# Performance work log

Measured on AMD Instinct MI355X. Metric: run time of the kernel, lower is better.

Reference implementation:

```python
import jax, jax.numpy as jnp
import numpy as np

B, S, D = 2, 2048, 2048
H, KVH = 32, 8
HD = D // H          # 64
N_REP = H // KVH     # 4
NEG = -1e9


def setup_inputs() -> dict:
    key = jax.random.key(0)
    ks = jax.random.split(key, 5)
    x = jax.random.normal(ks[0], (B, S, D), dtype=jnp.float32)
    std = 0.02
    wq = jax.random.normal(ks[1], (H * HD, D), dtype=jnp.float32) * std
    wk = jax.random.normal(ks[2], (KVH * HD, D), dtype=jnp.float32) * std
    wv = jax.random.normal(ks[3], (KVH * HD, D), dtype=jnp.float32) * std
    wo = jax.random.normal(ks[4], (D, H * HD), dtype=jnp.float32) * std
    # RoPE tables: (S, HD//2)
    inv_freq = 1.0 / (10000.0 ** (np.arange(0, HD, 2, dtype=np.float32) / HD))
    t = np.arange(S, dtype=np.float32)
    freqs = np.outer(t, inv_freq)
    freqs_cos = jnp.asarray(np.cos(freqs))
    freqs_sin = jnp.asarray(np.sin(freqs))
    # additive causal mask [1,1,S,S]
    causal = np.tril(np.ones((S, S), dtype=bool))
    mask = jnp.asarray(np.where(causal, 0.0, NEG).astype(np.float32))[None, None]
    return {"x": x, "wq": wq, "wk": wk, "wv": wv, "wo": wo,
            "freqs_cos": freqs_cos, "freqs_sin": freqs_sin, "mask": mask}


def _apply_rope(t, cos, sin):
    # t: [B,S,nh,HD]; cos/sin: [S, HD//2]
    tr = t.reshape(t.shape[:-1] + (HD // 2, 2))
    r, i = tr[..., 0], tr[..., 1]
    c = cos[None, :, None, :]
    s = sin[None, :, None, :]
    out_r = r * c - i * s
    out_i = r * s + i * c
    return jnp.stack([out_r, out_i], axis=-1).reshape(t.shape)


def reference(x, wq, wk, wv, wo, freqs_cos, freqs_sin, mask):
    b, s, _ = x.shape
    q = (x @ wq.T).reshape(b, s, H, HD)
    k = (x @ wk.T).reshape(b, s, KVH, HD)
    v = (x @ wv.T).reshape(b, s, KVH, HD)
    q = _apply_rope(q, freqs_cos, freqs_sin)
    k = _apply_rope(k, freqs_cos, freqs_sin)
    # repeat_kv (GQA expansion) then move heads forward: [B,H,S,HD]
    k = jnp.repeat(k, N_REP, axis=2)
    v = jnp.repeat(v, N_REP, axis=2)
    q = q.transpose(0, 2, 1, 3)
    k = k.transpose(0, 2, 1, 3)
    v = v.transpose(0, 2, 1, 3)
    scale = 1.0 / jnp.sqrt(jnp.float32(HD))
    scores = jnp.einsum("bhqd,bhkd->bhqk", q, k) * scale + mask[:, :, :s, :s]
    attn = jax.nn.softmax(scores, axis=-1)
    out = jnp.einsum("bhqk,bhkd->bhqd", attn, v)
    out = out.transpose(0, 2, 1, 3).reshape(b, s, H * HD)
    return out @ wo.T
```

## Files before the change

### kernel.cpp

```cpp
#include <hip/hip_runtime.h>
#include <hip/hip_bf16.h>
#include <stdint.h>


#define NEG_BIG (-1e9f)
#define SCALE_LOG2 0.18033688011112042f
#define DEFER_THR 10.0f

typedef __bf16 bf16x8 __attribute__((ext_vector_type(8)));
typedef float f32x4 __attribute__((ext_vector_type(4)));
typedef float f32x16 __attribute__((ext_vector_type(16)));
typedef uint16_t u16x8 __attribute__((ext_vector_type(8)));
typedef uint32_t u32x4 __attribute__((ext_vector_type(4)));

__device__ inline uint16_t f2bf(float x) {
    __hip_bfloat16 h = __float2bfloat16(x);
    return __builtin_bit_cast(uint16_t, h);
}
__device__ inline float bf2f(uint16_t u) {
    uint32_t t = (uint32_t)u << 16;
    return __builtin_bit_cast(float, t);
}

__device__ inline void async_cp16(const void* g, void* l) {
    __builtin_amdgcn_global_load_lds(
        (const __attribute__((address_space(1))) uint32_t*)g,
        (__attribute__((address_space(3))) uint32_t*)l,
        16 , 0 , 0 );
}

__global__ void cvt4(const float* __restrict__ in, uint16_t* __restrict__ out, int n4) {
    int i = blockIdx.x * blockDim.x + threadIdx.x;
    if (i >= n4) return;
    const float4 v = ((const float4*)in)[i];
    ushort4 o;
    o.x = f2bf(v.x); o.y = f2bf(v.y); o.z = f2bf(v.z); o.w = f2bf(v.w);
    ((ushort4*)out)[i] = o;
}

__global__ void build_wqkv(const float* __restrict__ wq, const float* __restrict__ wk,
                           const float* __restrict__ wv, uint16_t* __restrict__ out) {
    int i = blockIdx.x * blockDim.x + threadIdx.x;
    if (i >= (3072 * 2048) / 4) return;
    int e = i * 4;
    int row = e >> 11;
    int col = e & 2047;
    const float* src = (row < 2048) ? (wq + (long)row * 2048 + col)
                     : (row < 2560) ? (wk + (long)(row - 2048) * 2048 + col)
                                    : (wv + (long)(row - 2560) * 2048 + col);
    const float4 v = *(const float4*)src;
    ushort4 o;
    o.x = f2bf(v.x); o.y = f2bf(v.y); o.z = f2bf(v.z); o.w = f2bf(v.w);
    ((ushort4*)(out + e))[0] = o;
}

template <int OUT_BF16>
__global__ __launch_bounds__(256) void gemm_bt(const uint16_t* __restrict__ A,
                                               const uint16_t* __restrict__ Bw,
                                               void* __restrict__ Cout,
                                               int M, int N, int K) {
    __shared__ __align__(16) uint16_t Asm[128 * 32];
    __shared__ __align__(16) uint16_t Bsm[128 * 32];
    const int t = threadIdx.x;
    const int l = t & 63;
    const int w = t >> 6;
    const int wr = w >> 1, wc = w & 1;
    const int c = l & 15, g = l >> 4;
    const long row0 = (long)blockIdx.x * 128;
    const long col0 = (long)blockIdx.y * 128;

    f32x4 acc[4][4] = {};

    const uint16_t* aSrc = A + (row0 + (t >> 2)) * (long)K + (t & 3) * 8;
    const uint16_t* bSrc = Bw + (col0 + (t >> 2)) * (long)K + (t & 3) * 8;
    const long half = 64L * K;

    for (int k0 = 0; k0 < K; k0 += 32) {
        __syncthreads();
        async_cp16(aSrc + k0, &Asm[t * 8]);
        async_cp16(aSrc + half + k0, &Asm[2048 + t * 8]);
        async_cp16(bSrc + k0, &Bsm[t * 8]);
        async_cp16(bSrc + half + k0, &Bsm[2048 + t * 8]);
        __syncthreads();

        bf16x8 aF[4], bF[4];
        const int ko = g * 8;
#pragma unroll
        for (int m = 0; m < 4; ++m)
            aF[m] = *(const bf16x8*)&Asm[(wr * 64 + m * 16 + c) * 32 + ko];
#pragma unroll
        for (int n = 0; n < 4; ++n)
            bF[n] = *(const bf16x8*)&Bsm[(wc * 64 + n * 16 + c) * 32 + ko];
#pragma unroll
        for (int m = 0; m < 4; ++m)
#pragma unroll
            for (int n = 0; n < 4; ++n)
                acc[m][n] = __builtin_amdgcn_mfma_f32_16x16x32_bf16(aF[m], bF[n], acc[m][n], 0, 0, 0);
    }

#pragma unroll
    for (int m = 0; m < 4; ++m) {
        const long rg = row0 + wr * 64 + m * 16 + g * 4;
#pragma unroll
        for (int n = 0; n < 4; ++n) {
            const long cg = col0 + wc * 64 + n * 16 + c;
#pragma unroll
            for (int r = 0; r < 4; ++r) {
                float v = acc[m][n][r];
                if (OUT_BF16)
                    ((uint16_t*)Cout)[(rg + r) * (long)N + cg] = f2bf(v);
                else
                    ((float*)Cout)[(rg + r) * (long)N + cg] = v;
            }
        }
    }
}

__global__ void rope_q(uint16_t* __restrict__ qkv,
                       const float* __restrict__ cosT,
                       const float* __restrict__ sinT) {
    int idx = blockIdx.x * blockDim.x + threadIdx.x;
    if (idx >= 4096 * 1024) return;
    int m = idx >> 10;
    int j = idx & 1023;
    int s = m & 2047;
    int d2 = j & 31;
    float cc = cosT[s * 32 + d2];
    float ss = sinT[s * 32 + d2];
    uint32_t* p = (uint32_t*)(qkv + (long)m * 3072 + 2 * j);
    uint32_t v = *p;
    float re = bf2f((uint16_t)(v & 0xffffu));
    float im = bf2f((uint16_t)(v >> 16));
    float orr = re * cc - im * ss;
    float oi = re * ss + im * cc;
    *p = (uint32_t)f2bf(orr) | ((uint32_t)f2bf(oi) << 16);
}

__global__ void kpack_rope(const uint16_t* __restrict__ qkv,
                           const float* __restrict__ cosT,
                           const float* __restrict__ sinT,
                           uint16_t* __restrict__ Kpk) {
    const int wid = (blockIdx.x * blockDim.x + threadIdx.x) >> 6;
    const int l = threadIdx.x & 63;
    const int lq = l & 31, hi = l >> 5;
    const int s = wid & 3;
    const int tile = (wid >> 2) & 63;
    const int bk = wid >> 8;
    const int b = bk >> 3, kvh = bk & 7;
    const int key = 32 * tile + lq;
    const uint16_t* src = qkv + (long)(b * 2048 + key) * 3072
                        + 2048 + kvh * 64 + 16 * s + 8 * hi;
    u16x8 v = *(const u16x8*)src;
    const int d2b = 8 * s + 4 * hi;
    u16x8 o;
#pragma unroll
    for (int p = 0; p < 4; ++p) {
        const float cc = cosT[key * 32 + d2b + p];
        const float ss = sinT[key * 32 + d2b + p];
        const float re = bf2f(v[2 * p]);
        const float im = bf2f(v[2 * p + 1]);
        o[2 * p]     = f2bf(re * cc - im * ss);
        o[2 * p + 1] = f2bf(re * ss + im * cc);
    }
    *(u16x8*)(Kpk + (((long)(bk * 64 + tile) * 4 + s) * 64 + l) * 8) = o;
}

__global__ void vpack_direct(const uint16_t* __restrict__ qkv, uint16_t* __restrict__ Vpk) {
    const int wid = (blockIdx.x * blockDim.x + threadIdx.x) >> 6;
    const int l = threadIdx.x & 63;
    const int lq = l & 31, hi = l >> 5;
    const int s2 = wid & 1;
    const int nd = (wid >> 1) & 1;
    const int tile = (wid >> 2) & 63;
    const int bk = wid >> 8;
    const int b = bk >> 3, kvh = bk & 7;
    const int key0 = 32 * tile + 16 * s2 + 8 * hi;
    const uint16_t* src = qkv + (long)(b * 2048 + key0) * 3072
                        + 2560 + kvh * 64 + nd * 32 + lq;
    u16x8 v;
#pragma unroll
    for (int jj = 0; jj < 8; ++jj) v[jj] = src[(long)jj * 3072];
    *(u16x8*)(Vpk + ((((long)(bk * 64 + tile) * 2 + nd) * 2 + s2) * 64 + l) * 8) = v;
}

__device__ inline void pack_pf(const float pr[16], int hi, bf16x8 pf[2]) {
    uint32_t wds[8], xw[8];
#pragma unroll
    for (int m = 0; m < 8; ++m)
        wds[m] = (uint32_t)f2bf(pr[2 * m]) | ((uint32_t)f2bf(pr[2 * m + 1]) << 16);
#pragma unroll
    for (int m = 0; m < 8; ++m)
        xw[m] = (uint32_t)__shfl_xor((int)wds[m], 32);
#pragma unroll
    for (int s = 0; s < 2; ++s) {
        u32x4 pk;
        pk[0] = hi ? xw[4 * s + 2] : wds[4 * s + 0];
        pk[1] = hi ? xw[4 * s + 3] : wds[4 * s + 1];
        pk[2] = hi ? wds[4 * s + 2] : xw[4 * s + 0];
        pk[3] = hi ? wds[4 * s + 3] : xw[4 * s + 1];
        pf[s] = __builtin_bit_cast(bf16x8, pk);
    }
}

__global__ __launch_bounds__(128) void attn_fwd(const uint16_t* __restrict__ qkv,
                                                const uint16_t* __restrict__ Kpk,
                                                const uint16_t* __restrict__ Vpk,
                                                uint16_t* __restrict__ outb) {
    const int bid = blockIdx.x;
    const int bhp = bid & 31;
    const int j = 63 - (bid >> 5);
    const int t0 = threadIdx.x;
    const int l = t0 & 63, ww = t0 >> 6;
    const int gh = 2 * bhp + ww;
    const int b = gh >> 5, h = gh & 31;
    const int kvh = h >> 2;
    const int bk = b * 8 + kvh;
    const int lq = l & 31, hi = l >> 5;
    const int q = 32 * j + lq;

    const uint16_t* qrow = qkv + (long)(b * 2048 + q) * 3072 + h * 64 + 8 * hi;
    bf16x8 qf[4];
#pragma unroll
    for (int s = 0; s < 4; ++s) qf[s] = *(const bf16x8*)(qrow + 16 * s);

    float m_run = -1e30f, l_run = 0.f;
    f32x16 accO[2] = {};

    const uint16_t* kbase = Kpk + (long)bk * 64 * 2048 + (long)l * 8;
    const uint16_t* vbase = Vpk + (long)bk * 64 * 2048 + (long)l * 8;
    const int nT = (j + 2) >> 1;

    for (int t = 0; t < nT; ++t) {
        bf16x8 kf[2][4];
#pragma unroll
        for (int u = 0; u < 2; ++u)
#pragma unroll
            for (int s = 0; s < 4; ++s)
                kf[u][s] = *(const bf16x8*)(kbase + (long)(2 * t + u) * 2048 + s * 512);

        f32x16 st0 = {}, st1 = {};
        __builtin_amdgcn_s_setprio(1);
#pragma unroll
        for (int s = 0; s < 4; ++s)
            st0 = __builtin_amdgcn_mfma_f32_32x32x16_bf16(kf[0][s], qf[s], st0, 0, 0, 0);
#pragma unroll
        for (int s = 0; s < 4; ++s)
            st1 = __builtin_amdgcn_mfma_f32_32x32x16_bf16(kf[1][s], qf[s], st1, 0, 0, 0);
        __builtin_amdgcn_s_setprio(0);

        bf16x8 vf[2][2][2];
#pragma unroll
        for (int u = 0; u < 2; ++u)
#pragma unroll
            for (int nd = 0; nd < 2; ++nd)
#pragma unroll
                for (int s2 = 0; s2 < 2; ++s2)
                    vf[u][nd][s2] = *(const bf16x8*)(vbase + (long)(2 * t + u) * 2048 + nd * 1024 + s2 * 512);

        float sc0[16], sc1[16];
        if (t == nT - 1) {
            const int tq0 = lq + ((j - 2 * t) << 5) - 4 * hi;
            const int tq1 = tq0 - 32;
#pragma unroll
            for (int r = 0; r < 16; ++r) {
                const int kc = (r & 3) + 8 * (r >> 2);
                sc0[r] = st0[r] * SCALE_LOG2 + (kc > tq0 ? NEG_BIG : 0.f);
                sc1[r] = st1[r] * SCALE_LOG2 + (kc > tq1 ? NEG_BIG : 0.f);
            }
        } else {
#pragma unroll
            for (int r = 0; r < 16; ++r) {
                sc0[r] = st0[r] * SCALE_LOG2;
                sc1[r] = st1[r] * SCALE_LOG2;
            }
        }

        float vm = sc0[0];
#pragma unroll
        for (int r = 1; r < 16; ++r) vm = fmaxf(vm, sc0[r]);
#pragma unroll
        for (int r = 0; r < 16; ++r) vm = fmaxf(vm, sc1[r]);
        vm = fmaxf(vm, __shfl_xor(vm, 32));
        if (!__all(vm - m_run <= DEFER_THR)) {
            const float mnew = fmaxf(m_run, vm);
            const float alpha = __builtin_amdgcn_exp2f(m_run - mnew);
            m_run = mnew;
            l_run *= alpha;
#pragma unroll
            for (int nd = 0; nd < 2; ++nd)
#pragma unroll
                for (int r = 0; r < 16; ++r) accO[nd][r] *= alpha;
        }

        float pr0[16], pr1[16];
        float sum = 0.f;
#pragma unroll
        for (int r = 0; r < 16; ++r) {
            pr0[r] = __builtin_amdgcn_exp2f(sc0[r] - m_run);
            sum += pr0[r];
        }
#pragma unroll
        for (int r = 0; r < 16; ++r) {
            pr1[r] = __builtin_amdgcn_exp2f(sc1[r] - m_run);
            sum += pr1[r];
        }
        sum += __shfl_xor(sum, 32);
        l_run += sum;

        bf16x8 pf0[2], pf1[2];
        pack_pf(pr0, hi, pf0);
        pack_pf(pr1, hi, pf1);

        __builtin_amdgcn_s_setprio(1);
#pragma unroll
        for (int nd = 0; nd < 2; ++nd) {
            accO[nd] = __builtin_amdgcn_mfma_f32_32x32x16_bf16(vf[0][nd][0], pf0[0], accO[nd], 0, 0, 0);
            accO[nd] = __builtin_amdgcn_mfma_f32_32x32x16_bf16(vf[0][nd][1], pf0[1], accO[nd], 0, 0, 0);
            accO[nd] = __builtin_amdgcn_mfma_f32_32x32x16_bf16(vf[1][nd][0], pf1[0], accO[nd], 0, 0, 0);
            accO[nd] = __builtin_amdgcn_mfma_f32_32x32x16_bf16(vf[1][nd][1], pf1[1], accO[nd], 0, 0, 0);
        }
        __builtin_amdgcn_s_setprio(0);
    }

    const float invl = 1.0f / l_run;
    uint16_t* orow = outb + (long)(b * 2048 + q) * 2048 + h * 64 + 4 * hi;
#pragma unroll
    for (int nd = 0; nd < 2; ++nd)
#pragma unroll
        for (int m = 0; m < 4; ++m) {
            ushort4 o;
            o.x = f2bf(accO[nd][4 * m + 0] * invl);
            o.y = f2bf(accO[nd][4 * m + 1] * invl);
            o.z = f2bf(accO[nd][4 * m + 2] * invl);
            o.w = f2bf(accO[nd][4 * m + 3] * invl);
            *(ushort4*)(orow + nd * 32 + 8 * m) = o;
        }
}

extern "C" void kernel_launch(void* const* d_in, const int* in_sizes, int n_in,
                              void* d_out, int out_size, void* d_ws, size_t ws_size,
                              hipStream_t stream) {
    const float* x    = (const float*)d_in[0];
    const float* wq   = (const float*)d_in[1];
    const float* wk   = (const float*)d_in[2];
    const float* wv   = (const float*)d_in[3];
    const float* wo   = (const float*)d_in[4];
    const float* fcos = (const float*)d_in[5];
    const float* fsin = (const float*)d_in[6];
    float* out = (float*)d_out;

    uint8_t* ws = (uint8_t*)d_ws;
    const size_t MiB = 1048576;
    uint16_t* x_bf   = (uint16_t*)(ws);
    uint16_t* w_bf   = (uint16_t*)(ws + 16 * MiB);
    uint16_t* qkv_bf = (uint16_t*)(ws + 28 * MiB);
    uint16_t* att_bf = x_bf;
    uint16_t* Kpk    = (uint16_t*)(ws + 16 * MiB);
    uint16_t* Vpk    = (uint16_t*)(ws + 20 * MiB);
    uint16_t* wo_bf  = (uint16_t*)(ws + 16 * MiB);

    cvt4<<<(2097152 + 255) / 256, 256, 0, stream>>>(x, x_bf, 2097152);
    build_wqkv<<<(1572864 + 255) / 256, 256, 0, stream>>>(wq, wk, wv, w_bf);

    gemm_bt<1><<<dim3(32, 24), 256, 0, stream>>>(x_bf, w_bf, qkv_bf, 4096, 3072, 2048);

    rope_q<<<16384, 256, 0, stream>>>(qkv_bf, fcos, fsin);
    kpack_rope<<<1024, 256, 0, stream>>>(qkv_bf, fcos, fsin, Kpk);
    vpack_direct<<<1024, 256, 0, stream>>>(qkv_bf, Vpk);

    attn_fwd<<<2048, 128, 0, stream>>>(qkv_bf, Kpk, Vpk, att_bf);

    cvt4<<<(1048576 + 255) / 256, 256, 0, stream>>>(wo, wo_bf, 1048576);
    gemm_bt<0><<<dim3(32, 16), 256, 0, stream>>>(att_bf, wo_bf, out, 4096, 2048, 2048);
}
```

Before: 230.6 us.

## Prefetch K tiles with double buffering and fold softmax scale into Q RoPE

The attention loop now double-buffers K fragments, loading the next key tile before the current one is processed, so global-load latency overlaps with MFMA and softmax work. The softmax scale (log2e/sqrt(d)) moves into the Q RoPE kernel, which removes per-score multiplies. The masking uses direct assignment, and the max and sum reductions become tree-shaped with exp and bf16 packing fused. It also sets launch bounds to 4 blocks per CU and remaps block-to-head order for better KV locality. The cost is more register pressure from the second K buffer, plus an extra bf16 rounding of the scaled Q.

Result: slower. 380.2 us (+64.9%).

```diff
diff --git a/kernel.cpp b/kernel.cpp
--- a/kernel.cpp
+++ b/kernel.cpp
@@ -131,8 +131,8 @@
     uint32_t v = *p;
     float re = bf2f((uint16_t)(v & 0xffffu));
     float im = bf2f((uint16_t)(v >> 16));
-    float orr = re * cc - im * ss;
-    float oi = re * ss + im * cc;
+    float orr = (re * cc - im * ss) * SCALE_LOG2;
+    float oi  = (re * ss + im * cc) * SCALE_LOG2;
     *p = (uint32_t)f2bf(orr) | ((uint32_t)f2bf(oi) << 16);
 }
 
@@ -183,11 +183,8 @@
     *(u16x8*)(Vpk + ((((long)(bk * 64 + tile) * 2 + nd) * 2 + s2) * 64 + l) * 8) = v;
 }
 
-__device__ inline void pack_pf(const float pr[16], int hi, bf16x8 pf[2]) {
-    uint32_t wds[8], xw[8];
-#pragma unroll
-    for (int m = 0; m < 8; ++m)
-        wds[m] = (uint32_t)f2bf(pr[2 * m]) | ((uint32_t)f2bf(pr[2 * m + 1]) << 16);
+__device__ inline void pack_pf_w(const uint32_t wds[8], int hi, bf16x8 pf[2]) {
+    uint32_t xw[8];
 #pragma unroll
     for (int m = 0; m < 8; ++m)
         xw[m] = (uint32_t)__shfl_xor((int)wds[m], 32);
@@ -202,13 +199,14 @@
     }
 }
 
-__global__ __launch_bounds__(128) void attn_fwd(const uint16_t* __restrict__ qkv,
-                                                const uint16_t* __restrict__ Kpk,
-                                                const uint16_t* __restrict__ Vpk,
-                                                uint16_t* __restrict__ outb) {
+__global__ __launch_bounds__(128, 4) void attn_fwd(const uint16_t* __restrict__ qkv,
+                                                   const uint16_t* __restrict__ Kpk,
+                                                   const uint16_t* __restrict__ Vpk,
+                                                   uint16_t* __restrict__ outb) {
     const int bid = blockIdx.x;
-    const int bhp = bid & 31;
+    const int bhpp = bid & 31;
     const int j = 63 - (bid >> 5);
+    const int bhp = ((bhpp & 7) << 1) | ((bhpp >> 3) & 1) | (bhpp & 16);
     const int t0 = threadIdx.x;
     const int l = t0 & 63, ww = t0 >> 6;
     const int gh = 2 * bhp + ww;
@@ -230,14 +228,16 @@
     const uint16_t* vbase = Vpk + (long)bk * 64 * 2048 + (long)l * 8;
     const int nT = (j + 2) >> 1;
 
-    for (int t = 0; t < nT; ++t) {
-        bf16x8 kf[2][4];
+    auto LOADK = [&](bf16x8 (&kf)[2][4], int tt) {
+        const uint16_t* kp = kbase + (long)(2 * tt) * 2048;
 #pragma unroll
         for (int u = 0; u < 2; ++u)
 #pragma unroll
             for (int s = 0; s < 4; ++s)
-                kf[u][s] = *(const bf16x8*)(kbase + (long)(2 * t + u) * 2048 + s * 512);
-
+                kf[u][s] = *(const bf16x8*)(kp + u * 2048 + s * 512);
+    };
+
+    auto BODY = [&](bf16x8 (&kf)[2][4], int tt) {
         f32x16 st0 = {}, st1 = {};
         __builtin_amdgcn_s_setprio(1);
 #pragma unroll
@@ -248,6 +248,7 @@
             st1 = __builtin_amdgcn_mfma_f32_32x32x16_bf16(kf[1][s], qf[s], st1, 0, 0, 0);
         __builtin_amdgcn_s_setprio(0);
 
+        const uint16_t* vp = vbase + (long)(2 * tt) * 2048;
         bf16x8 vf[2][2][2];
 #pragma unroll
         for (int u = 0; u < 2; ++u)
@@ -255,32 +256,28 @@
             for (int nd = 0; nd < 2; ++nd)
 #pragma unroll
                 for (int s2 = 0; s2 < 2; ++s2)
-                    vf[u][nd][s2] = *(const bf16x8*)(vbase + (long)(2 * t + u) * 2048 + nd * 1024 + s2 * 512);
-
-        float sc0[16], sc1[16];
-        if (t == nT - 1) {
-            const int tq0 = lq + ((j - 2 * t) << 5) - 4 * hi;
+                    vf[u][nd][s2] = *(const bf16x8*)(vp + u * 2048 + nd * 1024 + s2 * 512);
+
+        if (tt == nT - 1) {
+            const int tq0 = lq + ((j - 2 * tt) << 5) - 4 * hi;
             const int tq1 = tq0 - 32;
 #pragma unroll
             for (int r = 0; r < 16; ++r) {
                 const int kc = (r & 3) + 8 * (r >> 2);
-                sc0[r] = st0[r] * SCALE_LOG2 + (kc > tq0 ? NEG_BIG : 0.f);
-                sc1[r] = st1[r] * SCALE_LOG2 + (kc > tq1 ? NEG_BIG : 0.f);
+                if (kc > tq0) st0[r] = NEG_BIG;
+                if (kc > tq1) st1[r] = NEG_BIG;
             }
-        } else {
-#pragma unroll
-            for (int r = 0; r < 16; ++r) {
-                sc0[r] = st0[r] * SCALE_LOG2;
-                sc1[r] = st1[r] * SCALE_LOG2;
-            }
-        }
-
-        float vm = sc0[0];
-#pragma unroll
-        for (int r = 1; r < 16; ++r) vm = fmaxf(vm, sc0[r]);
-#pragma unroll
-        for (int r = 0; r < 16; ++r) vm = fmaxf(vm, sc1[r]);
-        vm = fmaxf(vm, __shfl_xor(vm, 32));
+        }
+
+        float mx[16];
+#pragma unroll
+        for (int r = 0; r < 16; ++r) mx[r] = fmaxf(st0[r], st1[r]);
+#pragma unroll
+        for (int off = 8; off; off >>= 1)
+#pragma unroll
+            for (int r = 0; r < 8; ++r)
+                if (r < off) mx[r] = fmaxf(mx[r], mx[r + off]);
+        const float vm = fmaxf(mx[0], __shfl_xor(mx[0], 32));
         if (!__all(vm - m_run <= DEFER_THR)) {
             const float mnew = fmaxf(m_run, vm);
             const float alpha = __builtin_amdgcn_exp2f(m_run - mnew);
@@ -292,24 +289,29 @@
                 for (int r = 0; r < 16; ++r) accO[nd][r] *= alpha;
         }
 
-        float pr0[16], pr1[16];
-        float sum = 0.f;
-#pragma unroll
-        for (int r = 0; r < 16; ++r) {
-            pr0[r] = __builtin_amdgcn_exp2f(sc0[r] - m_run);
-            sum += pr0[r];
-        }
-#pragma unroll
-        for (int r = 0; r < 16; ++r) {
-            pr1[r] = __builtin_amdgcn_exp2f(sc1[r] - m_run);
-            sum += pr1[r];
-        }
-        sum += __shfl_xor(sum, 32);
+        uint32_t wds0[8], wds1[8];
+        float sm[8];
+#pragma unroll
+        for (int m = 0; m < 8; ++m) {
+            const float a0 = __builtin_amdgcn_exp2f(st0[2 * m] - m_run);
+            const float a1 = __builtin_amdgcn_exp2f(st0[2 * m + 1] - m_run);
+            const float b0 = __builtin_amdgcn_exp2f(st1[2 * m] - m_run);
+            const float b1 = __builtin_amdgcn_exp2f(st1[2 * m + 1] - m_run);
+            wds0[m] = (uint32_t)f2bf(a0) | ((uint32_t)f2bf(a1) << 16);
+            wds1[m] = (uint32_t)f2bf(b0) | ((uint32_t)f2bf(b1) << 16);
+            sm[m] = (a0 + a1) + (b0 + b1);
+        }
+#pragma unroll
+        for (int off = 4; off; off >>= 1)
+#pragma unroll
+            for (int r = 0; r < 4; ++r)
+                if (r < off) sm[r] += sm[r + off];
+        float sum = sm[0] + __shfl_xor(sm[0], 32);
         l_run += sum;
 
         bf16x8 pf0[2], pf1[2];
-        pack_pf(pr0, hi, pf0);
-        pack_pf(pr1, hi, pf1);
+        pack_pf_w(wds0, hi, pf0);
+        pack_pf_w(wds1, hi, pf1);
 
         __builtin_amdgcn_s_setprio(1);
 #pragma unroll
@@ -320,7 +322,19 @@
             accO[nd] = __builtin_amdgcn_mfma_f32_32x32x16_bf16(vf[1][nd][1], pf1[1], accO[nd], 0, 0, 0);
         }
         __builtin_amdgcn_s_setprio(0);
-    }
+    };
+
+    bf16x8 kA[2][4], kB[2][4];
+    LOADK(kA, 0);
+    int t = 0;
+#pragma unroll 1
+    for (; t + 1 < nT; t += 2) {
+        LOADK(kB, t + 1);
+        BODY(kA, t);
+        if (t + 2 < nT) LOADK(kA, t + 2);
+        BODY(kB, t + 1);
+    }
+    if (t < nT) BODY(kA, t);
 
     const float invl = 1.0f / l_run;
     uint16_t* orow = outb + (long)(b * 2048 + q) * 2048 + h * 64 + 4 * hi;
```

## Replace GEMM with 256-row double-buffered swizzled-LDS tiled kernel

Applied to the files above, without the earlier changes.

Replaces the 128x128 single-buffered GEMM with a 256xBN tile kernel using 512 threads, BK=64, double-buffered LDS staging with async copies overlapping the MFMA loop, and an XOR swizzle on LDS layout to avoid bank conflicts. It also raises wave priority around the MFMA bursts. Larger tiles increase operand reuse, but they use far more LDS (up to 128 KiB) and registers, which lowers occupancy. The QKV GEMM now launches only 192 blocks, which may underfill the GPU's compute units.

After: 221.9 us. 3.7% less time.

```diff
diff --git a/kernel.cpp b/kernel.cpp
--- a/kernel.cpp
+++ b/kernel.cpp
@@ -54,56 +54,92 @@
     ((ushort4*)(out + e))[0] = o;
 }
 
-template <int OUT_BF16>
-__global__ __launch_bounds__(256) void gemm_bt(const uint16_t* __restrict__ A,
+template <int BN, int OUT_BF16>
+__global__ __launch_bounds__(512) void gemm256(const uint16_t* __restrict__ A,
                                                const uint16_t* __restrict__ Bw,
                                                void* __restrict__ Cout,
                                                int M, int N, int K) {
-    __shared__ __align__(16) uint16_t Asm[128 * 32];
-    __shared__ __align__(16) uint16_t Bsm[128 * 32];
-    const int t = threadIdx.x;
-    const int l = t & 63;
-    const int w = t >> 6;
-    const int wr = w >> 1, wc = w & 1;
+    constexpr int WN = BN / 4;
+    constexpr int NF = WN / 16;
+    constexpr int BROUNDS = BN / 64;
+
+    __shared__ __align__(16) uint16_t As[2][256 * 64];
+    __shared__ __align__(16) uint16_t Bs[2][BN * 64];
+
+    const int tid = threadIdx.x;
+    const int l = tid & 63;
+    const int w = tid >> 6;
+    const int wmi = w >> 2;
+    const int wni = w & 3;
     const int c = l & 15, g = l >> 4;
-    const long row0 = (long)blockIdx.x * 128;
-    const long col0 = (long)blockIdx.y * 128;
-
-    f32x4 acc[4][4] = {};
-
-    const uint16_t* aSrc = A + (row0 + (t >> 2)) * (long)K + (t & 3) * 8;
-    const uint16_t* bSrc = Bw + (col0 + (t >> 2)) * (long)K + (t & 3) * 8;
-    const long half = 64L * K;
-
-    for (int k0 = 0; k0 < K; k0 += 32) {
-        __syncthreads();
-        async_cp16(aSrc + k0, &Asm[t * 8]);
-        async_cp16(aSrc + half + k0, &Asm[2048 + t * 8]);
-        async_cp16(bSrc + k0, &Bsm[t * 8]);
-        async_cp16(bSrc + half + k0, &Bsm[2048 + t * 8]);
-        __syncthreads();
-
-        bf16x8 aF[4], bF[4];
-        const int ko = g * 8;
-#pragma unroll
-        for (int m = 0; m < 4; ++m)
-            aF[m] = *(const bf16x8*)&Asm[(wr * 64 + m * 16 + c) * 32 + ko];
-#pragma unroll
-        for (int n = 0; n < 4; ++n)
-            bF[n] = *(const bf16x8*)&Bsm[(wc * 64 + n * 16 + c) * 32 + ko];
-#pragma unroll
-        for (int m = 0; m < 4; ++m)
-#pragma unroll
-            for (int n = 0; n < 4; ++n)
-                acc[m][n] = __builtin_amdgcn_mfma_f32_16x16x32_bf16(aF[m], bF[n], acc[m][n], 0, 0, 0);
+    const long row0 = (long)blockIdx.x * 256;
+    const long col0 = (long)blockIdx.y * BN;
+
+    f32x4 acc[8][NF] = {};
+
+    auto STAGE = [&](int buf, int t) {
+        const long k0 = (long)t * 64;
+#pragma unroll
+        for (int rr = 0; rr < 4; ++rr) {
+            const int e = rr * 512 + tid;
+            const int r = e >> 3;
+            const int gs = (e & 7) ^ (r & 7);
+            async_cp16(A + (row0 + r) * (long)K + k0 + gs * 8, &As[buf][e * 8]);
+        }
+#pragma unroll
+        for (int rr = 0; rr < BROUNDS; ++rr) {
+            const int e = rr * 512 + tid;
+            const int r = e >> 3;
+            const int gs = (e & 7) ^ (r & 7);
+            async_cp16(Bw + (col0 + r) * (long)K + k0 + gs * 8, &Bs[buf][e * 8]);
+        }
+    };
+
+    STAGE(0, 0);
+    __syncthreads();
+
+    const int nt = K / 64;
+    for (int t = 0; t < nt; ++t) {
+        const int cur = t & 1;
+        if (t + 1 < nt) STAGE(cur ^ 1, t + 1);
+
+#pragma unroll
+        for (int kk = 0; kk < 2; ++kk) {
+            bf16x8 bF[NF];
+#pragma unroll
+            for (int n = 0; n < NF; ++n) {
+                const int rb = wni * WN + n * 16 + c;
+                const int sp = ((kk * 4 + g) ^ (c & 7));
+                bF[n] = *(const bf16x8*)&Bs[cur][rb * 64 + sp * 8];
+            }
+#pragma unroll
+            for (int mh = 0; mh < 2; ++mh) {
+                bf16x8 aF[4];
+#pragma unroll
+                for (int mm = 0; mm < 4; ++mm) {
+                    const int ra = wmi * 128 + (mh * 4 + mm) * 16 + c;
+                    const int sp = ((kk * 4 + g) ^ (c & 7));
+                    aF[mm] = *(const bf16x8*)&As[cur][ra * 64 + sp * 8];
+                }
+                __builtin_amdgcn_s_setprio(1);
+#pragma unroll
+                for (int mm = 0; mm < 4; ++mm)
+#pragma unroll
+                    for (int n = 0; n < NF; ++n)
+                        acc[mh * 4 + mm][n] = __builtin_amdgcn_mfma_f32_16x16x32_bf16(
+                            aF[mm], bF[n], acc[mh * 4 + mm][n], 0, 0, 0);
+                __builtin_amdgcn_s_setprio(0);
+            }
+        }
+        if (t + 1 < nt) __syncthreads();
     }
 
 #pragma unroll
-    for (int m = 0; m < 4; ++m) {
-        const long rg = row0 + wr * 64 + m * 16 + g * 4;
-#pragma unroll
-        for (int n = 0; n < 4; ++n) {
-            const long cg = col0 + wc * 64 + n * 16 + c;
+    for (int m = 0; m < 8; ++m) {
+        const long rg = row0 + wmi * 128 + m * 16 + g * 4;
+#pragma unroll
+        for (int n = 0; n < NF; ++n) {
+            const long cg = col0 + wni * WN + n * 16 + c;
 #pragma unroll
             for (int r = 0; r < 4; ++r) {
                 float v = acc[m][n][r];
@@ -362,7 +398,7 @@
     cvt4<<<(2097152 + 255) / 256, 256, 0, stream>>>(x, x_bf, 2097152);
     build_wqkv<<<(1572864 + 255) / 256, 256, 0, stream>>>(wq, wk, wv, w_bf);
 
-    gemm_bt<1><<<dim3(32, 24), 256, 0, stream>>>(x_bf, w_bf, qkv_bf, 4096, 3072, 2048);
+    gemm256<256, 1><<<dim3(16, 12), 512, 0, stream>>>(x_bf, w_bf, qkv_bf, 4096, 3072, 2048);
 
     rope_q<<<16384, 256, 0, stream>>>(qkv_bf, fcos, fsin);
     kpack_rope<<<1024, 256, 0, stream>>>(qkv_bf, fcos, fsin, Kpk);
@@ -371,5 +407,5 @@
     attn_fwd<<<2048, 128, 0, stream>>>(qkv_bf, Kpk, Vpk, att_bf);
 
     cvt4<<<(1048576 + 255) / 256, 256, 0, stream>>>(wo, wo_bf, 1048576);
-    gemm_bt<0><<<dim3(32, 16), 256, 0, stream>>>(att_bf, wo_bf, out, 4096, 2048, 2048);
-}
+    gemm256<128, 0><<<dim3(16, 16), 512, 0, stream>>>(att_bf, wo_bf, out, 4096, 2048, 2048);
+}
```
